# Kernel tuning notes

Measured on AMD Instinct MI355X. Metric: run time of the kernel, lower is better.

The kernel has to match this reference:

```python
import jax, jax.numpy as jnp
import numpy as np

B, T, D, A = 16, 2048, 512, 64


def setup_inputs() -> dict:
    key = jax.random.key(0)
    ks = jax.random.split(key, 7)
    s = 1.0 / np.sqrt(D)
    return {
        "inp": jax.random.normal(ks[0], (B, T, D), dtype=jnp.float32),
        "Wq": jax.random.normal(ks[1], (D, A), dtype=jnp.float32) * s,
        "bq": jax.random.normal(ks[2], (A,), dtype=jnp.float32) * 0.01,
        "Wk": jax.random.normal(ks[3], (D, A), dtype=jnp.float32) * s,
        "bk": jax.random.normal(ks[4], (A,), dtype=jnp.float32) * 0.01,
        "Wv": jax.random.normal(ks[5], (D, A), dtype=jnp.float32) * s,
        "bv": jax.random.normal(ks[6], (A,), dtype=jnp.float32) * 0.01,
    }


def reference(inp, Wq, bq, Wk, bk, Wv, bv):
    # Projections: (B,T,D) @ (D,A) -> (B,T,A)
    Q = inp @ Wq + bq
    K = inp @ Wk + bk
    V = inp @ Wv + bv
    # Scaled QK^T: (B,T,T)
    scores = jnp.einsum("btd,bsd->bts", Q, K) / jnp.sqrt(jnp.float32(A))
    # Sign-based K padding mask: mask[b, s] = sign(|sum_a K[b,s,a]|)
    k_mask = jnp.sign(jnp.abs(K.sum(axis=-1)))  # (B,T)
    scores = jnp.where(k_mask[:, None, :] == 0, jnp.float32(1e-8), scores)
    att = jax.nn.softmax(scores, axis=-1)
    # Sign-based Q mask broadcast along the key axis (faithful to Mask module)
    q_mask = jnp.sign(jnp.abs(Q.sum(axis=-1)))  # (B,T)
    att = att * q_mask[:, None, :]
    # dropout_keep_prob == 1 -> dropout is identity
    ctx = jnp.einsum("bts,bsa->bta", att, V)  # (B,T,A)
    # inp^T @ ctx -> (B,D,A), then sum over A -> (B,D)
    out = jnp.einsum("btd,bta->bd", inp, ctx)
    return out
```

## Files before the change

kernel.cpp:

```cpp
#include <hip/hip_runtime.h>

#define B_ 16
#define T_ 2048
#define D_ 512
#define SCALE_LOG2E 0.18033688f

typedef __bf16 bf16x8 __attribute__((ext_vector_type(8)));
typedef float  f32x4  __attribute__((ext_vector_type(4)));

__device__ inline unsigned short f2bf(float f){
    union { float f; unsigned u; } x; x.f = f;
    unsigned r = x.u + 0x7fffu + ((x.u >> 16) & 1u);
    return (unsigned short)(r >> 16);
}

__device__ inline bf16x8 ldfrag(const unsigned short* p){
    uint4 v = *reinterpret_cast<const uint4*>(p);
    return __builtin_bit_cast(bf16x8, v);
}


__global__ void setup_kernel(const float* __restrict__ Wq, const float* __restrict__ Wk,
                             const float* __restrict__ Wv, const float* __restrict__ bq,
                             const float* __restrict__ bk, const float* __restrict__ bv,
                             unsigned short* __restrict__ WcT, float* __restrict__ bsum,
                             float* __restrict__ out)
{
    int e = blockIdx.x * 256 + threadIdx.x;
    if (e < 73728){
        int j = e >> 9, d = e & 511;
        float v;
        if (j < 64)       v = Wq[d * 64 + j];
        else if (j < 128) v = Wk[d * 64 + (j - 64)];
        else if (j < 131){
            const float* src = (j == 128) ? Wq : (j == 129) ? Wk : Wv;
            const float4* p = reinterpret_cast<const float4*>(&src[d * 64]);
            v = 0.f;
            #pragma unroll
            for (int i = 0; i < 16; i++){ float4 t = p[i]; v += (t.x + t.y) + (t.z + t.w); }
        }
        else v = 0.f;
        WcT[j * 512 + d] = f2bf(v);
    } else if (e < 73744){
        int mm = e - 73728;
        float s = 0.f;
        const float* src = (mm == 0) ? bq : (mm == 1) ? bk : bv;
        if (mm < 3){
            const float4* p = reinterpret_cast<const float4*>(src);
            #pragma unroll
            for (int i = 0; i < 16; i++){ float4 t = p[i]; s += (t.x + t.y) + (t.z + t.w); }
        }
        bsum[mm] = s;
    } else if (e < 81936){
        out[e - 73744] = 0.f;
    }
}

__global__ __launch_bounds__(256) void proj_kernel(
    const float* __restrict__ inp, const unsigned short* __restrict__ WcT,
    const float* __restrict__ bq, const float* __restrict__ bk,
    const float* __restrict__ bsum,
    unsigned short* __restrict__ Qb, unsigned short* __restrict__ Kb,
    float* __restrict__ wvp)
{
    __shared__ __align__(16) unsigned short Af[4 * 512];
    __shared__ __align__(16) unsigned short Bf[9 * 512];
    __shared__ float kzsh[64];
    const int tid  = threadIdx.x;
    const int r0   = blockIdx.x * 64;
    const int lane = tid & 63, wvid = tid >> 6;
    const int m = lane & 15, q = lane >> 4;
    const int mh = wvid >> 1, nh = wvid & 1;

    const int ar = tid >> 2, aseg = tid & 3;
    unsigned short* a_dst = &Af[(ar >> 4) * 512 + (aseg * 16 + (ar & 15)) * 8];
    const float* a_src = &inp[(size_t)(r0 + ar) * 512 + aseg * 8];
    const unsigned short* b_src0 = &WcT[(((tid      ) >> 6) * 16 + (tid & 15)) * 512 + ((tid >> 4) & 3) * 8];
    const unsigned short* b_src1 = &WcT[(((tid + 256) >> 6) * 16 + (tid & 15)) * 512 + ((tid >> 4) & 3) * 8];
    const unsigned short* b_src2 = &WcT[(((tid + 512) >> 6) * 16 + (tid & 15)) * 512 + ((tid >> 4) & 3) * 8];
    uint4* b_dst0 = reinterpret_cast<uint4*>(&Bf[(tid      ) * 8]);
    uint4* b_dst1 = reinterpret_cast<uint4*>(&Bf[(tid + 256) * 8]);
    uint4* b_dst2 = reinterpret_cast<uint4*>(&Bf[(tid + 512) * 8]);

    f32x4 acc[5][2];
    #pragma unroll
    for (int t = 0; t < 5; t++){
        acc[t][0] = (f32x4){0.f, 0.f, 0.f, 0.f};
        acc[t][1] = (f32x4){0.f, 0.f, 0.f, 0.f};
    }

    float4 ga0 = *reinterpret_cast<const float4*>(a_src);
    float4 ga1 = *reinterpret_cast<const float4*>(a_src + 4);
    uint4 gb0 = *reinterpret_cast<const uint4*>(b_src0);
    uint4 gb1 = *reinterpret_cast<const uint4*>(b_src1);
    uint4 gb2 = (tid < 64) ? *reinterpret_cast<const uint4*>(b_src2) : (uint4){0,0,0,0};

    const int ntile = 5 - nh;
    const int tbase = nh * 5;

    for (int kk = 0; kk < 512; kk += 32){
        uint4 pk;
        pk.x = f2bf(ga0.x) | ((unsigned)f2bf(ga0.y) << 16);
        pk.y = f2bf(ga0.z) | ((unsigned)f2bf(ga0.w) << 16);
        pk.z = f2bf(ga1.x) | ((unsigned)f2bf(ga1.y) << 16);
        pk.w = f2bf(ga1.z) | ((unsigned)f2bf(ga1.w) << 16);
        *reinterpret_cast<uint4*>(a_dst) = pk;
        *b_dst0 = gb0;
        *b_dst1 = gb1;
        if (tid < 64) *b_dst2 = gb2;
        __syncthreads();
        if (kk < 480){
            ga0 = *reinterpret_cast<const float4*>(a_src + kk + 32);
            ga1 = *reinterpret_cast<const float4*>(a_src + kk + 36);
            gb0 = *reinterpret_cast<const uint4*>(b_src0 + kk + 32);
            gb1 = *reinterpret_cast<const uint4*>(b_src1 + kk + 32);
            if (tid < 64) gb2 = *reinterpret_cast<const uint4*>(b_src2 + kk + 32);
        }
        bf16x8 a0 = ldfrag(&Af[(mh * 2    ) * 512 + lane * 8]);
        bf16x8 a1 = ldfrag(&Af[(mh * 2 + 1) * 512 + lane * 8]);
        #pragma unroll
        for (int t = 0; t < 5; t++){
            if (t < ntile){
                bf16x8 bfr = ldfrag(&Bf[(tbase + t) * 512 + lane * 8]);
                acc[t][0] = __builtin_amdgcn_mfma_f32_16x16x32_bf16(a0, bfr, acc[t][0], 0, 0, 0);
                acc[t][1] = __builtin_amdgcn_mfma_f32_16x16x32_bf16(a1, bfr, acc[t][1], 0, 0, 0);
            }
        }
        __syncthreads();
    }

    if (nh == 1){
        const float bs = bsum[m];
        #pragma unroll
        for (int f = 0; f < 2; f++){
            #pragma unroll
            for (int i = 0; i < 4; i++){
                int rl = mh * 32 + f * 16 + q * 4 + i;
                float val = acc[3][f][i] + bs;
                float qsv = __shfl(val, (lane & 48));
                float ksv = __shfl(val, (lane & 48) | 1);
                float vsv = __shfl(val, (lane & 48) | 2);
                if (m == 0){
                    kzsh[rl] = (ksv == 0.f) ? 0.f : 1.f;
                    wvp[(size_t)r0 + rl] = (qsv == 0.f) ? 0.f : vsv;
                }
            }
        }
    }
    __syncthreads();

    if (nh == 0){
        float bqv[4];
        #pragma unroll
        for (int t = 0; t < 4; t++) bqv[t] = bq[t * 16 + m];
        const float bkv0 = bk[m];
        #pragma unroll
        for (int f = 0; f < 2; f++){
            #pragma unroll
            for (int i = 0; i < 4; i++){
                int rl = mh * 32 + f * 16 + q * 4 + i;
                size_t r = (size_t)r0 + rl;
                float kz = kzsh[rl];
                #pragma unroll
                for (int t = 0; t < 4; t++)
                    Qb[r * 64 + t * 16 + m] = f2bf((acc[t][f][i] + bqv[t]) * SCALE_LOG2E);
                Kb[r * 64 + m] = f2bf((acc[4][f][i] + bkv0) * kz);
            }
        }
    } else {
        float bkv[3];
        #pragma unroll
        for (int t = 0; t < 3; t++) bkv[t] = bk[16 + t * 16 + m];
        #pragma unroll
        for (int f = 0; f < 2; f++){
            #pragma unroll
            for (int i = 0; i < 4; i++){
                int rl = mh * 32 + f * 16 + q * 4 + i;
                size_t r = (size_t)r0 + rl;
                float kz = kzsh[rl];
                #pragma unroll
                for (int t = 0; t < 3; t++)
                    Kb[r * 64 + 16 + t * 16 + m] = f2bf((acc[t][f][i] + bkv[t]) * kz);
            }
        }
    }
}

__global__ __launch_bounds__(512) void attn_out_kernel(
    const float* __restrict__ inp,
    const unsigned short* __restrict__ Qb, const unsigned short* __restrict__ Kb,
    const float* __restrict__ wvp, float* __restrict__ out)
{
    __shared__ __align__(16) unsigned short Kf[2][8 * 512];
    __shared__ float csh[128];
    const int tid = threadIdx.x;
    const int lane = tid & 63, wvid = tid >> 6;
    const int m = lane & 15, q = lane >> 4;
    const int b  = blockIdx.y;
    const int t0 = blockIdx.x * 128;
    const size_t base = (size_t)b * T_;

    const unsigned short* qp = &Qb[(base + t0 + wvid * 16 + m) * 64 + q * 8];
    bf16x8 a0 = ldfrag(qp), a1 = ldfrag(qp + 32);

    const unsigned short* ksrc = &Kb[(base + (wvid >> 1) * 16 + m) * 64 + (wvid & 1) * 32 + q * 8];
    const int k_off = wvid * 512 + lane * 8;
    uint4 stg = *reinterpret_cast<const uint4*>(ksrc);

    float num[4] = {0,0,0,0}, den[4] = {0,0,0,0};

    for (int it = 0; it < 32; it++){
        const int p = it & 1;
        *reinterpret_cast<uint4*>(&Kf[p][k_off]) = stg;
        __syncthreads();
        if (it < 31) stg = *reinterpret_cast<const uint4*>(ksrc + (it + 1) * 4096);
        float w[4];
        #pragma unroll
        for (int st = 0; st < 4; st++) w[st] = wvp[base + it * 64 + st * 16 + m];
        #pragma unroll
        for (int st = 0; st < 4; st++){
            bf16x8 b0 = ldfrag(&Kf[p][(st * 2    ) * 512 + lane * 8]);
            bf16x8 b1 = ldfrag(&Kf[p][(st * 2 + 1) * 512 + lane * 8]);
            f32x4 z = (f32x4){0.f,0.f,0.f,0.f};
            z = __builtin_amdgcn_mfma_f32_16x16x32_bf16(a0, b0, z, 0, 0, 0);
            z = __builtin_amdgcn_mfma_f32_16x16x32_bf16(a1, b1, z, 0, 0, 0);
            float wst = w[st];
            #pragma unroll
            for (int i = 0; i < 4; i++){
                float e = exp2f(z[i]);
                den[i] += e;
                num[i] = fmaf(e, wst, num[i]);
            }
        }
    }
    #pragma unroll
    for (int s = 1; s < 16; s <<= 1){
        #pragma unroll
        for (int i = 0; i < 4; i++){
            num[i] += __shfl_xor(num[i], s);
            den[i] += __shfl_xor(den[i], s);
        }
    }
    __syncthreads();
    if (m == 0){
        #pragma unroll
        for (int i = 0; i < 4; i++)
            csh[wvid * 16 + q * 4 + i] = num[i] / den[i];
    }
    __syncthreads();

    const float* ip = inp + (base + t0) * 512 + tid;
    float a = 0.f;
    #pragma unroll 8
    for (int t = 0; t < 128; t++)
        a = fmaf(ip[(size_t)t * 512], csh[t], a);
    atomicAdd(&out[b * 512 + tid], a);
}

extern "C" void kernel_launch(void* const* d_in, const int* in_sizes, int n_in,
                              void* d_out, int out_size, void* d_ws, size_t ws_size,
                              hipStream_t stream)
{
    const float* inp = (const float*)d_in[0];
    const float* Wq  = (const float*)d_in[1];
    const float* bq  = (const float*)d_in[2];
    const float* Wk  = (const float*)d_in[3];
    const float* bk  = (const float*)d_in[4];
    const float* Wv  = (const float*)d_in[5];
    const float* bv  = (const float*)d_in[6];
    float* out = (float*)d_out;

    char* ws = (char*)d_ws;
    unsigned short* WcT = (unsigned short*)(ws);
    float* bsum         = (float*)(ws + 147456);
    unsigned short* Qb  = (unsigned short*)(ws + 262144);
    unsigned short* Kb  = (unsigned short*)(ws + 4456448);
    float* wvp          = (float*)(ws + 8650752);

    setup_kernel<<<321, 256, 0, stream>>>(Wq, Wk, Wv, bq, bk, bv, WcT, bsum, out);
    proj_kernel<<<512, 256, 0, stream>>>(inp, WcT, bq, bk, bsum, Qb, Kb, wvp);
    attn_out_kernel<<<dim3(16, 16), 512, 0, stream>>>(inp, Qb, Kb, wvp, out);
}
```

Measured before the change: 152.8 us.

## Rewrite projection kernel to load MFMA fragments directly from global memory per wave

```diff
diff --git a/kernel.cpp b/kernel.cpp
--- a/kernel.cpp
+++ b/kernel.cpp
@@ -63,126 +63,69 @@
     unsigned short* __restrict__ Qb, unsigned short* __restrict__ Kb,
     float* __restrict__ wvp)
 {
-    __shared__ __align__(16) unsigned short Af[4 * 512];
-    __shared__ __align__(16) unsigned short Bf[9 * 512];
-    __shared__ float kzsh[64];
     const int tid  = threadIdx.x;
-    const int r0   = blockIdx.x * 64;
     const int lane = tid & 63, wvid = tid >> 6;
     const int m = lane & 15, q = lane >> 4;
-    const int mh = wvid >> 1, nh = wvid & 1;
-
-    const int ar = tid >> 2, aseg = tid & 3;
-    unsigned short* a_dst = &Af[(ar >> 4) * 512 + (aseg * 16 + (ar & 15)) * 8];
-    const float* a_src = &inp[(size_t)(r0 + ar) * 512 + aseg * 8];
-    const unsigned short* b_src0 = &WcT[(((tid      ) >> 6) * 16 + (tid & 15)) * 512 + ((tid >> 4) & 3) * 8];
-    const unsigned short* b_src1 = &WcT[(((tid + 256) >> 6) * 16 + (tid & 15)) * 512 + ((tid >> 4) & 3) * 8];
-    const unsigned short* b_src2 = &WcT[(((tid + 512) >> 6) * 16 + (tid & 15)) * 512 + ((tid >> 4) & 3) * 8];
-    uint4* b_dst0 = reinterpret_cast<uint4*>(&Bf[(tid      ) * 8]);
-    uint4* b_dst1 = reinterpret_cast<uint4*>(&Bf[(tid + 256) * 8]);
-    uint4* b_dst2 = reinterpret_cast<uint4*>(&Bf[(tid + 512) * 8]);
-
-    f32x4 acc[5][2];
-    #pragma unroll
-    for (int t = 0; t < 5; t++){
-        acc[t][0] = (f32x4){0.f, 0.f, 0.f, 0.f};
-        acc[t][1] = (f32x4){0.f, 0.f, 0.f, 0.f};
-    }
-
-    float4 ga0 = *reinterpret_cast<const float4*>(a_src);
-    float4 ga1 = *reinterpret_cast<const float4*>(a_src + 4);
-    uint4 gb0 = *reinterpret_cast<const uint4*>(b_src0);
-    uint4 gb1 = *reinterpret_cast<const uint4*>(b_src1);
-    uint4 gb2 = (tid < 64) ? *reinterpret_cast<const uint4*>(b_src2) : (uint4){0,0,0,0};
-
-    const int ntile = 5 - nh;
-    const int tbase = nh * 5;
-
-    for (int kk = 0; kk < 512; kk += 32){
-        uint4 pk;
-        pk.x = f2bf(ga0.x) | ((unsigned)f2bf(ga0.y) << 16);
-        pk.y = f2bf(ga0.z) | ((unsigned)f2bf(ga0.w) << 16);
-        pk.z = f2bf(ga1.x) | ((unsigned)f2bf(ga1.y) << 16);
-        pk.w = f2bf(ga1.z) | ((unsigned)f2bf(ga1.w) << 16);
-        *reinterpret_cast<uint4*>(a_dst) = pk;
-        *b_dst0 = gb0;
-        *b_dst1 = gb1;
-        if (tid < 64) *b_dst2 = gb2;
-        __syncthreads();
-        if (kk < 480){
-            ga0 = *reinterpret_cast<const float4*>(a_src + kk + 32);
-            ga1 = *reinterpret_cast<const float4*>(a_src + kk + 36);
-            gb0 = *reinterpret_cast<const uint4*>(b_src0 + kk + 32);
-            gb1 = *reinterpret_cast<const uint4*>(b_src1 + kk + 32);
-            if (tid < 64) gb2 = *reinterpret_cast<const uint4*>(b_src2 + kk + 32);
-        }
-        bf16x8 a0 = ldfrag(&Af[(mh * 2    ) * 512 + lane * 8]);
-        bf16x8 a1 = ldfrag(&Af[(mh * 2 + 1) * 512 + lane * 8]);
-        #pragma unroll
-        for (int t = 0; t < 5; t++){
-            if (t < ntile){
-                bf16x8 bfr = ldfrag(&Bf[(tbase + t) * 512 + lane * 8]);
-                acc[t][0] = __builtin_amdgcn_mfma_f32_16x16x32_bf16(a0, bfr, acc[t][0], 0, 0, 0);
-                acc[t][1] = __builtin_amdgcn_mfma_f32_16x16x32_bf16(a1, bfr, acc[t][1], 0, 0, 0);
-            }
-        }
-        __syncthreads();
-    }
-
-    if (nh == 1){
-        const float bs = bsum[m];
-        #pragma unroll
-        for (int f = 0; f < 2; f++){
-            #pragma unroll
-            for (int i = 0; i < 4; i++){
-                int rl = mh * 32 + f * 16 + q * 4 + i;
-                float val = acc[3][f][i] + bs;
-                float qsv = __shfl(val, (lane & 48));
-                float ksv = __shfl(val, (lane & 48) | 1);
-                float vsv = __shfl(val, (lane & 48) | 2);
-                if (m == 0){
-                    kzsh[rl] = (ksv == 0.f) ? 0.f : 1.f;
-                    wvp[(size_t)r0 + rl] = (qsv == 0.f) ? 0.f : vsv;
-                }
-            }
-        }
-    }
-    __syncthreads();
-
-    if (nh == 0){
-        float bqv[4];
-        #pragma unroll
-        for (int t = 0; t < 4; t++) bqv[t] = bq[t * 16 + m];
-        const float bkv0 = bk[m];
-        #pragma unroll
-        for (int f = 0; f < 2; f++){
-            #pragma unroll
-            for (int i = 0; i < 4; i++){
-                int rl = mh * 32 + f * 16 + q * 4 + i;
-                size_t r = (size_t)r0 + rl;
-                float kz = kzsh[rl];
-                #pragma unroll
-                for (int t = 0; t < 4; t++)
-                    Qb[r * 64 + t * 16 + m] = f2bf((acc[t][f][i] + bqv[t]) * SCALE_LOG2E);
-                Kb[r * 64 + m] = f2bf((acc[4][f][i] + bkv0) * kz);
-            }
-        }
-    } else {
-        float bkv[3];
-        #pragma unroll
-        for (int t = 0; t < 3; t++) bkv[t] = bk[16 + t * 16 + m];
-        #pragma unroll
-        for (int f = 0; f < 2; f++){
-            #pragma unroll
-            for (int i = 0; i < 4; i++){
-                int rl = mh * 32 + f * 16 + q * 4 + i;
-                size_t r = (size_t)r0 + rl;
-                float kz = kzsh[rl];
-                #pragma unroll
-                for (int t = 0; t < 3; t++)
-                    Kb[r * 64 + 16 + t * 16 + m] = f2bf((acc[t][f][i] + bkv[t]) * kz);
-            }
-        }
+    const int r0 = blockIdx.x * 64 + wvid * 16;
+
+    const float* ap = &inp[(size_t)(r0 + m) * 512 + q * 8];
+    const unsigned short* bp = &WcT[m * 512 + q * 8];
+
+    f32x4 acc[9];
+    #pragma unroll
+    for (int t = 0; t < 9; t++) acc[t] = (f32x4){0.f, 0.f, 0.f, 0.f};
+
+    float4 f0 = *reinterpret_cast<const float4*>(ap);
+    float4 f1 = *reinterpret_cast<const float4*>(ap + 4);
+    uint4 bfr[9];
+    #pragma unroll
+    for (int t = 0; t < 9; t++) bfr[t] = *reinterpret_cast<const uint4*>(bp + t * 8192);
+
+    for (int it = 0; it < 16; it++){
+        uint4 au;
+        au.x = f2bf(f0.x) | ((unsigned)f2bf(f0.y) << 16);
+        au.y = f2bf(f0.z) | ((unsigned)f2bf(f0.w) << 16);
+        au.z = f2bf(f1.x) | ((unsigned)f2bf(f1.y) << 16);
+        au.w = f2bf(f1.z) | ((unsigned)f2bf(f1.w) << 16);
+        bf16x8 a = __builtin_bit_cast(bf16x8, au);
+        uint4 bcur[9];
+        #pragma unroll
+        for (int t = 0; t < 9; t++) bcur[t] = bfr[t];
+        if (it < 15){
+            const int kn = (it + 1) * 32;
+            f0 = *reinterpret_cast<const float4*>(ap + kn);
+            f1 = *reinterpret_cast<const float4*>(ap + kn + 4);
+            #pragma unroll
+            for (int t = 0; t < 9; t++)
+                bfr[t] = *reinterpret_cast<const uint4*>(bp + t * 8192 + kn);
+        }
+        #pragma unroll
+        for (int t = 0; t < 9; t++)
+            acc[t] = __builtin_amdgcn_mfma_f32_16x16x32_bf16(
+                         a, __builtin_bit_cast(bf16x8, bcur[t]), acc[t], 0, 0, 0);
+    }
+
+    float bqv[4], bkv[4];
+    #pragma unroll
+    for (int t = 0; t < 4; t++){ bqv[t] = bq[t * 16 + m]; bkv[t] = bk[t * 16 + m]; }
+    const float bs = bsum[m];
+
+    #pragma unroll
+    for (int i = 0; i < 4; i++){
+        size_t r = (size_t)r0 + q * 4 + i;
+        float val = acc[8][i] + bs;
+        float qsv = __shfl(val, (lane & 48));
+        float ksv = __shfl(val, (lane & 48) | 1);
+        float vsv = __shfl(val, (lane & 48) | 2);
+        float kz  = (ksv == 0.f) ? 0.f : 1.f;
+        #pragma unroll
+        for (int t = 0; t < 4; t++)
+            Qb[r * 64 + t * 16 + m] = f2bf((acc[t][i] + bqv[t]) * SCALE_LOG2E);
+        #pragma unroll
+        for (int t = 0; t < 4; t++)
+            Kb[r * 64 + t * 16 + m] = f2bf((acc[t + 4][i] + bkv[t]) * kz);
+        if (m == 0)
+            wvp[r] = (qsv == 0.f) ? 0.f : vsv;
     }
 }
 
```

Result: slower. 171.1 us (+12.0%).
